# Kernel optimization log

Hardware: AMD Instinct MI355X
Metric: run time of the kernel (lower is better)

Reference implementation:

```python
import jax, jax.numpy as jnp
import numpy as np

B, N, C = 4, 16384, 512
HEADS = 16
HEADC = C // HEADS
HIDDEN = int(C * 4.0)


def setup_inputs() -> dict:
    key = jax.random.key(0)
    ks = jax.random.split(key, 8)
    s1 = 1.0 / np.sqrt(C)
    s2 = 1.0 / np.sqrt(HIDDEN)
    return {
        "x": jax.random.normal(ks[0], (B, N, C), jnp.float32),
        "mask_matrix": jnp.zeros((1,), jnp.int32),
        "norm1_w": jnp.ones((C,), jnp.float32),
        "norm1_b": jnp.zeros((C,), jnp.float32),
        "kln_w": jnp.ones((HEADS, 1, HEADC), jnp.float32),
        "kln_b": jnp.zeros((HEADS, 1, HEADC), jnp.float32),
        "vln_w": jnp.ones((HEADS, 1, HEADC), jnp.float32),
        "vln_b": jnp.zeros((HEADS, 1, HEADC), jnp.float32),
        "norm2_w": jnp.ones((C,), jnp.float32),
        "norm2_b": jnp.zeros((C,), jnp.float32),
        "fc1_w": jax.random.uniform(ks[1], (HIDDEN, C), jnp.float32, -s1, s1),
        "fc1_b": jax.random.uniform(ks[2], (HIDDEN,), jnp.float32, -s1, s1),
        "fc2_w": jax.random.uniform(ks[3], (C, HIDDEN), jnp.float32, -s2, s2),
        "fc2_b": jax.random.uniform(ks[4], (C,), jnp.float32, -s2, s2),
    }


def _ln(t, w, b, eps=1e-5):
    # standard nn.LayerNorm: biased variance, eps inside sqrt
    mean = t.mean(-1, keepdims=True)
    var = ((t - mean) ** 2).mean(-1, keepdims=True)
    return w * (t - mean) / jnp.sqrt(var + eps) + b


def _ln_std(t, w, b, eps=1e-5):
    # custom LayerNorm: unbiased std (torch.std), eps added to std
    d = t.shape[-1]
    mean = t.mean(-1, keepdims=True)
    var = ((t - mean) ** 2).sum(-1, keepdims=True) / (d - 1)
    return w * ((t - mean) / (jnp.sqrt(var) + eps)) + b


def reference(x, mask_matrix, norm1_w, norm1_b, kln_w, kln_b, vln_w, vln_b,
              norm2_w, norm2_b, fc1_w, fc1_b, fc2_w, fc2_b):
    b, n, c = x.shape
    shortcut = x
    h = _ln(x, norm1_w, norm1_b)
    # simple_attn (softmax-free linear attention)
    qkv = h.reshape(b, n, HEADS, HEADC).transpose(0, 2, 1, 3)  # [B,H,N,D]
    q = qkv
    k = _ln_std(qkv, kln_w, kln_b)
    v = _ln_std(qkv, vln_w, vln_b)
    kv = jnp.einsum('bhnd,bhne->bhde', k, v) / n        # [B,H,D,D]
    attn = jnp.einsum('bhnd,bhde->bhne', q, kv)          # [B,H,N,D]
    attn = attn.transpose(0, 2, 1, 3).reshape(b, n, c)
    h = attn + h                                          # residual inside simple_attn (bias = x post-norm1)
    x = shortcut + h
    # MLP branch
    m = _ln(x, norm2_w, norm2_b)
    m = jax.nn.gelu(m @ fc1_w.T + fc1_b, approximate=False)
    m = m @ fc2_w.T + fc2_b
    return x + m
```

## Files before the change

### kernel.cpp

```cpp
#include <hip/hip_runtime.h>
#include <cstdint>

#define BB 4
#define NN 16384
#define CC 512
#define HH 16
#define DD 32
#define HID 2048
#define MTOT (BB * NN)

typedef __bf16 bf16_t;
typedef __bf16 bf16x8 __attribute__((ext_vector_type(8)));
typedef __bf16 bf16x4 __attribute__((ext_vector_type(4)));
typedef float  f32x4  __attribute__((ext_vector_type(4)));

__device__ __forceinline__ void gload_lds16(const void* g, void* l) {
  auto gp = reinterpret_cast<const __attribute__((address_space(1))) char*>(
      reinterpret_cast<uintptr_t>(g));
  auto lp = reinterpret_cast<__attribute__((address_space(3))) char*>(
      reinterpret_cast<uintptr_t>(l));
  __builtin_amdgcn_global_load_lds(gp, lp, 16, 0, 0);
}

__global__ __launch_bounds__(256) void cvt_bf16_kernel(const float* __restrict__ src,
                                                       bf16_t* __restrict__ dst) {
  const long i = ((long)blockIdx.x * 256 + threadIdx.x) * 4;
  const f32x4 v = *(const f32x4*)(src + i);
  bf16x4 o;
  o[0] = (bf16_t)v[0]; o[1] = (bf16_t)v[1]; o[2] = (bf16_t)v[2]; o[3] = (bf16_t)v[3];
  *(bf16x4*)(dst + i) = o;
}

__global__ __launch_bounds__(256) void norm1_kernel(const float* __restrict__ x,
                                                    const float* __restrict__ w,
                                                    const float* __restrict__ bvec,
                                                    bf16_t* __restrict__ h) {
  const int wv = threadIdx.x >> 6, l = threadIdx.x & 63;
  const long tok = (long)blockIdx.x * 4 + wv;
  const int c0 = l * 8;
  const f32x4 a = *(const f32x4*)(x + tok * CC + c0);
  const f32x4 b = *(const f32x4*)(x + tok * CC + c0 + 4);
  float v[8];
#pragma unroll
  for (int i = 0; i < 4; ++i) { v[i] = a[i]; v[4 + i] = b[i]; }
  float s = 0.f, s2 = 0.f;
#pragma unroll
  for (int i = 0; i < 8; ++i) { s += v[i]; s2 += v[i] * v[i]; }
  for (int off = 32; off; off >>= 1) { s += __shfl_xor(s, off); s2 += __shfl_xor(s2, off); }
  const float mean = s * (1.f / CC);
  const float var  = fmaxf(s2 * (1.f / CC) - mean * mean, 0.f);
  const float rstd = rsqrtf(var + 1e-5f);
  const f32x4 w0 = *(const f32x4*)(w + c0), w1 = *(const f32x4*)(w + c0 + 4);
  const f32x4 b0 = *(const f32x4*)(bvec + c0), b1 = *(const f32x4*)(bvec + c0 + 4);
  bf16x8 o;
#pragma unroll
  for (int i = 0; i < 4; ++i) {
    o[i]     = (bf16_t)(w0[i] * (v[i] - mean) * rstd + b0[i]);
    o[4 + i] = (bf16_t)(w1[i] * (v[4 + i] - mean) * rstd + b1[i]);
  }
  *(bf16x8*)(h + tok * CC + c0) = o;
}

__global__ __launch_bounds__(256) void kv_partial_kernel(const bf16_t* __restrict__ h,
                                                         const float* __restrict__ klw,
                                                         const float* __restrict__ klb,
                                                         const float* __restrict__ vlw,
                                                         const float* __restrict__ vlb,
                                                         float* __restrict__ kvp) {
  __shared__ bf16_t kb[256 * 32];
  __shared__ bf16_t vb[256 * 32];
  __shared__ float scratch[192 * 16];
  const int tid = threadIdx.x;
  const int bh = blockIdx.x >> 6, chunk = blockIdx.x & 63;
  const int head = bh & 15;
  const int b = bh >> 4;
  const long tok0 = ((long)b << 14) + chunk * 256;
  const bf16_t* src = h + (tok0 + tid) * (long)CC + head * DD;
  float hv[32];
  {
    float s = 0.f, s2 = 0.f;
#pragma unroll
    for (int c = 0; c < 4; ++c) {
      const bf16x8 r = *(const bf16x8*)(src + c * 8);
#pragma unroll
      for (int j = 0; j < 8; ++j) {
        hv[c * 8 + j] = (float)r[j]; s += hv[c * 8 + j]; s2 += hv[c * 8 + j] * hv[c * 8 + j];
      }
    }
    const float mean = s * (1.f / 32.f);
    const float varu = fmaxf((s2 - 32.f * mean * mean) * (1.f / 31.f), 0.f);
    const float inv = 1.f / (sqrtf(varu) + 1e-5f);
    const int sx = (tid >> 1) & 3;
#pragma unroll
    for (int c = 0; c < 4; ++c) {
      bf16x8 kc, vc;
#pragma unroll
      for (int j = 0; j < 8; ++j) {
        const int d = c * 8 + j;
        const float t = (hv[d] - mean) * inv;
        kc[j] = (bf16_t)(klw[head * DD + d] * t + klb[head * DD + d]);
        vc[j] = (bf16_t)(vlw[head * DD + d] * t + vlb[head * DD + d]);
      }
      *(bf16x8*)((char*)kb + tid * 64 + ((c ^ sx) * 16)) = kc;
      *(bf16x8*)((char*)vb + tid * 64 + ((c ^ sx) * 16)) = vc;
    }
  }
  __syncthreads();
  const int g = tid >> 6, l = tid & 63;
  const int d0 = (l >> 3) * 4, e0 = (l & 7) * 4;
  const int ck = (l >> 3) >> 1, hk = (l >> 3) & 1;
  const int ce = (l & 7) >> 1, he = l & 1;
  float a[4][4] = {};
  for (int t = g; t < 256; t += 4) {
    const int tx = (t >> 1) & 3;
    const bf16x4 kq = *(const bf16x4*)((const char*)kb + t * 64 + ((ck ^ tx) * 16) + hk * 8);
    const bf16x4 vq = *(const bf16x4*)((const char*)vb + t * 64 + ((ce ^ tx) * 16) + he * 8);
    float kf[4], vf[4];
#pragma unroll
    for (int i2 = 0; i2 < 4; ++i2) { kf[i2] = (float)kq[i2]; vf[i2] = (float)vq[i2]; }
#pragma unroll
    for (int i2 = 0; i2 < 4; ++i2)
#pragma unroll
      for (int j2 = 0; j2 < 4; ++j2) a[i2][j2] += kf[i2] * vf[j2];
  }
  __syncthreads();
  if (g) {
#pragma unroll
    for (int i2 = 0; i2 < 4; ++i2)
#pragma unroll
      for (int j2 = 0; j2 < 4; ++j2)
        scratch[((g - 1) * 64 + l) * 16 + i2 * 4 + j2] = a[i2][j2];
  }
  __syncthreads();
  if (!g) {
#pragma unroll
    for (int gg = 0; gg < 3; ++gg)
#pragma unroll
      for (int i2 = 0; i2 < 4; ++i2)
#pragma unroll
        for (int j2 = 0; j2 < 4; ++j2)
          a[i2][j2] += scratch[(gg * 64 + l) * 16 + i2 * 4 + j2];
    float* dst = kvp + ((long)(bh * 64 + chunk) << 10);
#pragma unroll
    for (int i2 = 0; i2 < 4; ++i2) {
      f32x4 st;
      st[0] = a[i2][0]; st[1] = a[i2][1]; st[2] = a[i2][2]; st[3] = a[i2][3];
      *(f32x4*)&dst[(d0 + i2) * 32 + e0] = st;
    }
  }
}

__global__ __launch_bounds__(256) void kv_reduce_kernel(const float* __restrict__ kvp,
                                                        bf16_t* __restrict__ kvT) {
  const int bh = blockIdx.x;
  const int i4 = threadIdx.x * 4;
  const int d = i4 >> 5, e0 = i4 & 31;
  float s[4] = {};
  const float* p = kvp + ((long)bh << 16) + i4;
  for (int ch = 0; ch < 64; ++ch) {
    const f32x4 t = *(const f32x4*)(p + (ch << 10));
    s[0] += t[0]; s[1] += t[1]; s[2] += t[2]; s[3] += t[3];
  }
  const float sc = 1.f / (float)NN;
  bf16_t* q = kvT + ((long)bh << 10);
#pragma unroll
  for (int j = 0; j < 4; ++j) q[(e0 + j) * 32 + d] = (bf16_t)(s[j] * sc);
}

#define ASTRIDE 520
__global__ __launch_bounds__(256) void attn_fused_kernel(const float* __restrict__ x,
                                                         const bf16_t* __restrict__ h,
                                                         const bf16_t* __restrict__ kvTg,
                                                         const float* __restrict__ n2w,
                                                         const float* __restrict__ n2b,
                                                         float* __restrict__ xout,
                                                         bf16_t* __restrict__ mout) {
  __shared__ bf16_t attn_s[32 * ASTRIDE];
  const int tid = threadIdx.x;
  const int wv = tid >> 6, lane = tid & 63;
  const int lr = lane & 15, kg = lane >> 4;
  const long tok0 = (long)blockIdx.x * 32;
  const int b = (int)(tok0 >> 14);
  const bf16_t* kvsrc = kvTg + ((long)b << 14);

  {
    const int tt = wv & 1, hh = wv >> 1;
    const bf16_t* arow = h + (tok0 + tt * 16 + lr) * (long)CC + kg * 8;
    const f32x4 zero = {};
#pragma unroll
    for (int hi = 0; hi < 8; ++hi) {
      const int hd = hh * 8 + hi;
      const bf16_t* kvh = kvsrc + (hd << 10) + kg * 8;
      const bf16x8 af = *(const bf16x8*)(arow + hd * DD);
      const bf16x8 b0 = *(const bf16x8*)(kvh + lr * 32);
      const bf16x8 b1 = *(const bf16x8*)(kvh + (16 + lr) * 32);
      const f32x4 a0 = __builtin_amdgcn_mfma_f32_16x16x32_bf16(af, b0, zero, 0, 0, 0);
      const f32x4 a1 = __builtin_amdgcn_mfma_f32_16x16x32_bf16(af, b1, zero, 0, 0, 0);
      const int rbase = tt * 16 + kg * 4;
#pragma unroll
      for (int rg = 0; rg < 4; ++rg) {
        attn_s[(rbase + rg) * ASTRIDE + hd * 32 + lr]      = (bf16_t)a0[rg];
        attn_s[(rbase + rg) * ASTRIDE + hd * 32 + 16 + lr] = (bf16_t)a1[rg];
      }
    }
  }
  __syncthreads();

  const int c0 = lane * 8;
  const f32x4 w0 = *(const f32x4*)(n2w + c0), w1 = *(const f32x4*)(n2w + c0 + 4);
  const f32x4 bb0 = *(const f32x4*)(n2b + c0), bb1 = *(const f32x4*)(n2b + c0 + 4);
  for (int it = 0; it < 8; ++it) {
    const int tl = wv * 8 + it;
    const long tok = tok0 + tl;
    const f32x4 xa = *(const f32x4*)(x + tok * CC + c0);
    const f32x4 xb = *(const f32x4*)(x + tok * CC + c0 + 4);
    const bf16x8 hv = *(const bf16x8*)(h + tok * CC + c0);
    const bf16x8 av = *(const bf16x8*)&attn_s[tl * ASTRIDE + c0];
    float x2[8];
#pragma unroll
    for (int i = 0; i < 4; ++i) {
      x2[i]     = xa[i] + (float)hv[i]     + (float)av[i];
      x2[4 + i] = xb[i] + (float)hv[4 + i] + (float)av[4 + i];
    }
    float s = 0.f, s2 = 0.f;
#pragma unroll
    for (int i = 0; i < 8; ++i) { s += x2[i]; s2 += x2[i] * x2[i]; }
    for (int off = 32; off; off >>= 1) { s += __shfl_xor(s, off); s2 += __shfl_xor(s2, off); }
    const float mean = s * (1.f / CC);
    const float var  = fmaxf(s2 * (1.f / CC) - mean * mean, 0.f);
    const float rstd = rsqrtf(var + 1e-5f);
    f32x4 oa, ob;
    bf16x8 om;
#pragma unroll
    for (int i = 0; i < 4; ++i) {
      oa[i] = x2[i]; ob[i] = x2[4 + i];
      om[i]     = (bf16_t)(w0[i] * (x2[i] - mean) * rstd + bb0[i]);
      om[4 + i] = (bf16_t)(w1[i] * (x2[4 + i] - mean) * rstd + bb1[i]);
    }
    *(f32x4*)(xout + tok * CC + c0) = oa;
    *(f32x4*)(xout + tok * CC + c0 + 4) = ob;
    *(bf16x8*)(mout + tok * CC + c0) = om;
  }
}

template <int K, int NOUT, bool GELU>
__global__ __launch_bounds__(256, 3) void gemm97_kernel(const bf16_t* __restrict__ A,
                                                        const bf16_t* __restrict__ Bw,
                                                        const float* __restrict__ bias,
                                                        bf16_t* __restrict__ outb,
                                                        float* __restrict__ outf) {
  constexpr int NTILE = NOUT / 128;
  constexpr int NT = K / 32;
  __shared__ char lds[32768];
  char* As = lds;
  char* Bs = lds + 8192;

  const int tid = threadIdx.x;
  const int wid = tid >> 6, lane = tid & 63;
  const int wr = wid >> 1, wc = wid & 1;
  const int lr = lane & 15, kg = lane >> 4;

  int bid = blockIdx.x;
  const int qq = gridDim.x >> 3;
  bid = (bid & 7) * qq + (bid >> 3);
  const long row0 = (long)(bid / NTILE) * 128;
  const long col0 = (long)(bid % NTILE) * 128;

  const int srow = tid >> 2;
  const int sce = (((tid & 3) ^ ((srow >> 1) & 3)) << 3);
  const bf16_t* gA = A + (row0 + srow) * (long)K + sce;
  const bf16_t* gB = Bw + (col0 + srow) * (long)K + sce;

  f32x4 acc[4][4] = {};

  const int cx = ((kg ^ ((lr >> 1) & 3)) << 4);
  const char* aB = As + (wr * 64 + lr) * 64 + cx;
  const char* bB = Bs + (wc * 64 + lr) * 64 + cx;

  for (int kt = 0; kt < NT; ++kt) {
    gload_lds16(gA + kt * 32, As + tid * 16);
    gload_lds16(gA + 64L * K + kt * 32, As + 4096 + tid * 16);
    gload_lds16(gB + kt * 32, Bs + tid * 16);
    gload_lds16(gB + 64L * K + kt * 32, Bs + 4096 + tid * 16);
    __syncthreads();
    bf16x8 af[4], bf[4];
#pragma unroll
    for (int m = 0; m < 4; ++m) af[m] = *(const bf16x8*)(aB + m * 1024);
#pragma unroll
    for (int n = 0; n < 4; ++n) bf[n] = *(const bf16x8*)(bB + n * 1024);
#pragma unroll
    for (int m = 0; m < 4; ++m)
#pragma unroll
      for (int n = 0; n < 4; ++n)
        acc[m][n] = __builtin_amdgcn_mfma_f32_16x16x32_bf16(af[m], bf[n], acc[m][n], 0, 0, 0);
    __syncthreads();
  }

  if constexpr (GELU) {
    bf16_t* ot = (bf16_t*)lds;
#pragma unroll
    for (int n = 0; n < 4; ++n) {
      const int col = wc * 64 + n * 16 + lr;
      const float bs = bias[col0 + col];
#pragma unroll
      for (int m = 0; m < 4; ++m) {
#pragma unroll
        for (int rg = 0; rg < 4; ++rg) {
          const int row = wr * 64 + m * 16 + kg * 4 + rg;
          const float v = acc[m][n][rg] + bs;
          const float u = 0.7978845608028654f * (v + 0.044715f * v * v * v);
          const float gv = v / (1.f + __expf(-2.f * u));
          const int ch = (col >> 3) ^ ((row >> 2) & 3);
          ot[row * 128 + ch * 8 + (col & 7)] = (bf16_t)gv;
        }
      }
    }
    __syncthreads();
#pragma unroll
    for (int it2 = 0; it2 < 8; ++it2) {
      const int idx = it2 * 256 + tid;
      const int row = idx >> 4, ch = idx & 15;
      const int chs = ch ^ ((row >> 2) & 3);
      const bf16x8 vv = *(const bf16x8*)&ot[row * 128 + chs * 8];
      *(bf16x8*)(outb + (row0 + row) * NOUT + col0 + ch * 8) = vv;
    }
  } else {
#pragma unroll
    for (int n = 0; n < 4; ++n) {
      const long col = col0 + wc * 64 + n * 16 + lr;
      const float bs = bias[col];
#pragma unroll
      for (int m = 0; m < 4; ++m) {
#pragma unroll
        for (int rg = 0; rg < 4; ++rg) {
          const long row = row0 + wr * 64 + m * 16 + kg * 4 + rg;
          outf[row * NOUT + col] += acc[m][n][rg] + bs;
        }
      }
    }
  }
}

extern "C" void kernel_launch(void* const* d_in, const int* in_sizes, int n_in,
                              void* d_out, int out_size, void* d_ws, size_t ws_size,
                              hipStream_t stream) {
  const float* x   = (const float*)d_in[0];
  const float* n1w = (const float*)d_in[2];
  const float* n1b = (const float*)d_in[3];
  const float* klw = (const float*)d_in[4];
  const float* klb = (const float*)d_in[5];
  const float* vlw = (const float*)d_in[6];
  const float* vlb = (const float*)d_in[7];
  const float* n2w = (const float*)d_in[8];
  const float* n2b = (const float*)d_in[9];
  const float* w1f = (const float*)d_in[10];
  const float* b1  = (const float*)d_in[11];
  const float* w2f = (const float*)d_in[12];
  const float* b2  = (const float*)d_in[13];
  float* out = (float*)d_out;

  int nch;
  if (ws_size >= 289538048ULL) nch = 2;
  else                         nch = 4;
  const long mch = MTOT / nch;

  char* ws = (char*)d_ws;
  size_t off = 0;
  bf16_t* h   = (bf16_t*)(ws + off); off += (size_t)MTOT * CC * 2;
  bf16_t* mb  = (bf16_t*)(ws + off); off += (size_t)MTOT * CC * 2;
  bf16_t* act = (bf16_t*)(ws + off); off += (size_t)mch * HID * 2;
  bf16_t* w1  = (bf16_t*)(ws + off); off += (size_t)HID * CC * 2;
  bf16_t* w2  = (bf16_t*)(ws + off); off += (size_t)HID * CC * 2;
  float*  kvp = (float*)(ws + off);  off += (size_t)BB * HH * 64 * 1024 * 4;
  bf16_t* kvT = (bf16_t*)(ws + off);

  cvt_bf16_kernel<<<1024, 256, 0, stream>>>(w1f, w1);
  cvt_bf16_kernel<<<1024, 256, 0, stream>>>(w2f, w2);
  norm1_kernel<<<MTOT / 4, 256, 0, stream>>>(x, n1w, n1b, h);
  kv_partial_kernel<<<BB * HH * 64, 256, 0, stream>>>(h, klw, klb, vlw, vlb, kvp);
  kv_reduce_kernel<<<BB * HH, 256, 0, stream>>>(kvp, kvT);
  attn_fused_kernel<<<MTOT / 32, 256, 0, stream>>>(x, h, kvT, n2w, n2b, out, mb);
  for (int ch = 0; ch < nch; ++ch) {
    gemm97_kernel<CC, HID, true>
        <<<(int)((mch / 128) * (HID / 128)), 256, 0, stream>>>(
        mb + (size_t)ch * mch * CC, w1, b1, act, nullptr);
    gemm97_kernel<HID, CC, false>
        <<<(int)((mch / 128) * (CC / 128)), 256, 0, stream>>>(
        act, w2, b2, nullptr, out + (size_t)ch * mch * CC);
  }
}
```

Before: 663.0 us.

## Replace MLP GEMMs with multi-stage pipelined kernel covering several column tiles per block

Replaces the single-buffered GEMM with a 5-buffer LDS ring whose async global-to-LDS loads run four stages ahead, gated by explicit vmcnt waits, so loads overlap with MFMA work. Each block now walks several 128-column tiles in sequence, 8 for fc1 and 4 for fc2, cutting the grid size and reusing the same A row strip. The LDS-staged coalesced GELU store is replaced by direct scattered bf16 stores, and occupancy drops to 2 blocks per SM because of the larger LDS. Fewer blocks and uncoalesced stores may offset the pipelining benefit.

```diff
diff --git a/kernel.cpp b/kernel.cpp
--- a/kernel.cpp
+++ b/kernel.cpp
@@ -243,17 +243,17 @@
   }
 }
 
-template <int K, int NOUT, bool GELU>
-__global__ __launch_bounds__(256, 3) void gemm97_kernel(const bf16_t* __restrict__ A,
-                                                        const bf16_t* __restrict__ Bw,
-                                                        const float* __restrict__ bias,
-                                                        bf16_t* __restrict__ outb,
-                                                        float* __restrict__ outf) {
+template <int K, int NOUT, int TPB, bool GELU>
+__global__ __launch_bounds__(256, 2) void gemm_pipe_kernel(const bf16_t* __restrict__ A,
+                                                           const bf16_t* __restrict__ Bw,
+                                                           const float* __restrict__ bias,
+                                                           bf16_t* __restrict__ outb,
+                                                           float* __restrict__ outf) {
+  constexpr int NTK = K / 32;
+  constexpr int STOT = TPB * NTK;
   constexpr int NTILE = NOUT / 128;
-  constexpr int NT = K / 32;
-  __shared__ char lds[32768];
-  char* As = lds;
-  char* Bs = lds + 8192;
+  constexpr int BPS = NTILE / TPB;
+  __shared__ char lds[5 * 16384];
 
   const int tid = threadIdx.x;
   const int wid = tid >> 6, lane = tid & 63;
@@ -263,26 +263,46 @@
   int bid = blockIdx.x;
   const int qq = gridDim.x >> 3;
   bid = (bid & 7) * qq + (bid >> 3);
-  const long row0 = (long)(bid / NTILE) * 128;
-  const long col0 = (long)(bid % NTILE) * 128;
+  const int strip = bid / BPS;
+  const int ct0 = (bid % BPS) * TPB;
+  const long row0 = (long)strip * 128;
 
   const int srow = tid >> 2;
   const int sce = (((tid & 3) ^ ((srow >> 1) & 3)) << 3);
   const bf16_t* gA = A + (row0 + srow) * (long)K + sce;
-  const bf16_t* gB = Bw + (col0 + srow) * (long)K + sce;
+
+  const int cx = ((kg ^ ((lr >> 1) & 3)) << 4);
+  const char* aBb = (const char*)lds + (wr * 64 + lr) * 64 + cx;
+  const char* bBb = (const char*)lds + 8192 + (wc * 64 + lr) * 64 + cx;
 
   f32x4 acc[4][4] = {};
 
-  const int cx = ((kg ^ ((lr >> 1) & 3)) << 4);
-  const char* aB = As + (wr * 64 + lr) * 64 + cx;
-  const char* bB = Bs + (wc * 64 + lr) * 64 + cx;
-
-  for (int kt = 0; kt < NT; ++kt) {
-    gload_lds16(gA + kt * 32, As + tid * 16);
-    gload_lds16(gA + 64L * K + kt * 32, As + 4096 + tid * 16);
-    gload_lds16(gB + kt * 32, Bs + tid * 16);
-    gload_lds16(gB + 64L * K + kt * 32, Bs + 4096 + tid * 16);
-    __syncthreads();
+  auto STAGE = [&](int s) {
+    const int tp = s / NTK, kt = s % NTK, buf = s % 5;
+    char* d = (char*)lds + buf * 16384 + tid * 16;
+    const bf16_t* ga = gA + kt * 32;
+    gload_lds16(ga, d);
+    gload_lds16(ga + 64L * K, d + 4096);
+    const bf16_t* gb = Bw + ((long)(ct0 + tp) * 128 + srow) * K + sce + kt * 32;
+    gload_lds16(gb, d + 8192);
+    gload_lds16(gb + 64L * K, d + 12288);
+  };
+
+  STAGE(0); STAGE(1); STAGE(2); STAGE(3);
+
+#pragma unroll 5
+  for (int s = 0; s < STOT; ++s) {
+    if (s + 4 < STOT) STAGE(s + 4);
+    const int rem = STOT - 1 - s;
+    if (rem >= 4)      asm volatile("s_waitcnt vmcnt(16)" ::: "memory");
+    else if (rem == 3) asm volatile("s_waitcnt vmcnt(12)" ::: "memory");
+    else if (rem == 2) asm volatile("s_waitcnt vmcnt(8)" ::: "memory");
+    else if (rem == 1) asm volatile("s_waitcnt vmcnt(4)" ::: "memory");
+    else               asm volatile("s_waitcnt vmcnt(0)" ::: "memory");
+    __builtin_amdgcn_s_barrier();
+    const int buf = s % 5;
+    const char* aB = aBb + buf * 16384;
+    const char* bB = bBb + buf * 16384;
     bf16x8 af[4], bf[4];
 #pragma unroll
     for (int m = 0; m < 4; ++m) af[m] = *(const bf16x8*)(aB + m * 1024);
@@ -293,50 +313,34 @@
 #pragma unroll
       for (int n = 0; n < 4; ++n)
         acc[m][n] = __builtin_amdgcn_mfma_f32_16x16x32_bf16(af[m], bf[n], acc[m][n], 0, 0, 0);
-    __syncthreads();
-  }
-
-  if constexpr (GELU) {
-    bf16_t* ot = (bf16_t*)lds;
-#pragma unroll
-    for (int n = 0; n < 4; ++n) {
-      const int col = wc * 64 + n * 16 + lr;
-      const float bs = bias[col0 + col];
-#pragma unroll
-      for (int m = 0; m < 4; ++m) {
-#pragma unroll
-        for (int rg = 0; rg < 4; ++rg) {
-          const int row = wr * 64 + m * 16 + kg * 4 + rg;
-          const float v = acc[m][n][rg] + bs;
-          const float u = 0.7978845608028654f * (v + 0.044715f * v * v * v);
-          const float gv = v / (1.f + __expf(-2.f * u));
-          const int ch = (col >> 3) ^ ((row >> 2) & 3);
-          ot[row * 128 + ch * 8 + (col & 7)] = (bf16_t)gv;
+    __builtin_amdgcn_s_barrier();
+    if ((s % NTK) == NTK - 1) {
+      const long col0 = (long)(ct0 + s / NTK) * 128;
+#pragma unroll
+      for (int n = 0; n < 4; ++n) {
+        const long col = col0 + wc * 64 + n * 16 + lr;
+        const float bs = bias[col];
+#pragma unroll
+        for (int m = 0; m < 4; ++m) {
+#pragma unroll
+          for (int rg = 0; rg < 4; ++rg) {
+            const long row = row0 + wr * 64 + m * 16 + kg * 4 + rg;
+            const float v = acc[m][n][rg] + bs;
+            if constexpr (GELU) {
+              const float u = 0.7978845608028654f * (v + 0.044715f * v * v * v);
+              const float gv = v / (1.f + __expf(-2.f * u));
+              outb[row * NOUT + col] = (bf16_t)gv;
+            } else {
+              outf[row * NOUT + col] += v;
+            }
+          }
         }
       }
-    }
-    __syncthreads();
-#pragma unroll
-    for (int it2 = 0; it2 < 8; ++it2) {
-      const int idx = it2 * 256 + tid;
-      const int row = idx >> 4, ch = idx & 15;
-      const int chs = ch ^ ((row >> 2) & 3);
-      const bf16x8 vv = *(const bf16x8*)&ot[row * 128 + chs * 8];
-      *(bf16x8*)(outb + (row0 + row) * NOUT + col0 + ch * 8) = vv;
-    }
-  } else {
-#pragma unroll
-    for (int n = 0; n < 4; ++n) {
-      const long col = col0 + wc * 64 + n * 16 + lr;
-      const float bs = bias[col];
-#pragma unroll
-      for (int m = 0; m < 4; ++m) {
-#pragma unroll
-        for (int rg = 0; rg < 4; ++rg) {
-          const long row = row0 + wr * 64 + m * 16 + kg * 4 + rg;
-          outf[row * NOUT + col] += acc[m][n][rg] + bs;
-        }
-      }
+#pragma unroll
+      for (int m = 0; m < 4; ++m)
+#pragma unroll
+        for (int n = 0; n < 4; ++n)
+          acc[m][n] = f32x4{};
     }
   }
 }
@@ -381,11 +385,11 @@
   kv_reduce_kernel<<<BB * HH, 256, 0, stream>>>(kvp, kvT);
   attn_fused_kernel<<<MTOT / 32, 256, 0, stream>>>(x, h, kvT, n2w, n2b, out, mb);
   for (int ch = 0; ch < nch; ++ch) {
-    gemm97_kernel<CC, HID, true>
-        <<<(int)((mch / 128) * (HID / 128)), 256, 0, stream>>>(
+    gemm_pipe_kernel<CC, HID, 8, true>
+        <<<(int)((mch / 128) * 2), 256, 0, stream>>>(
         mb + (size_t)ch * mch * CC, w1, b1, act, nullptr);
-    gemm97_kernel<HID, CC, false>
-        <<<(int)((mch / 128) * (CC / 128)), 256, 0, stream>>>(
+    gemm_pipe_kernel<HID, CC, 4, false>
+        <<<(int)(mch / 128), 256, 0, stream>>>(
         act, w2, b2, nullptr, out + (size_t)ch * mch * CC);
   }
 }
```

New measurement: 729.8 us. +10.1%, slower.
